# Kernel tuning notes

Measured on AMD Instinct MI355X. Metric: run time of the kernel, lower is better.

## Reference

```python
import jax, jax.numpy as jnp
import numpy as np

H = 16          # num_heads
WIN = 512       # window_size


def setup_inputs() -> dict:
    key = jax.random.key(0)
    ks = jax.random.split(key, 4)
    B, S, D = 1, 4096, 1024
    s = 1.0 / np.sqrt(D)
    x = jax.random.normal(ks[0], (B, S, D), jnp.float32)
    Wqkv = jax.random.normal(ks[1], (3 * D, D), jnp.float32) * s
    bqkv = jnp.zeros((3 * D,), jnp.float32)
    Wout = jax.random.normal(ks[2], (D, D), jnp.float32) * s
    bout = jnp.zeros((D,), jnp.float32)
    return {"x": x, "Wqkv": Wqkv, "bqkv": bqkv, "Wout": Wout, "bout": bout}


def reference(x, Wqkv, bqkv, Wout, bout):
    B, S, D = x.shape
    d = D // H
    pads = WIN // 2
    C = WIN                 # chunk of query tokens processed together
    N = S // C              # number of chunks
    L = C + WIN - 1         # key-block length covering all windows in a chunk

    qkv = (x @ Wqkv.T + bqkv).reshape(B, S, 3, H, d).transpose(2, 0, 3, 1, 4)
    q, k, v = qkv[0], qkv[1], qkv[2]          # [B,H,S,d]

    # zero-pad K/V exactly like F.pad(..., value=0.0) in the original
    kp = jnp.pad(k, ((0, 0), (0, 0), (pads, pads), (0, 0)))
    vp = jnp.pad(v, ((0, 0), (0, 0), (pads, pads), (0, 0)))

    # gather overlapping key/value blocks: chunk n covers padded idx [n*C, n*C+L)
    idx = jnp.arange(N)[:, None] * C + jnp.arange(L)[None, :]   # [N,L]
    kb = kp[:, :, idx, :]                      # [B,H,N,L,d]
    vb = vp[:, :, idx, :]
    qc = q.reshape(B, H, N, C, d)

    scores = jnp.einsum('bhncd,bhnld->bhncl', qc, kb) / np.sqrt(d).astype(np.float32)
    c = jnp.arange(C)[:, None]
    j = jnp.arange(L)[None, :]
    band = (j >= c) & (j < c + WIN)            # [C,L]; zero-pad keys stay IN (score 0), matching original
    scores = jnp.where(band, scores, -jnp.inf)
    attn = jax.nn.softmax(scores, axis=-1)

    o = jnp.einsum('bhncl,bhnld->bhncd', attn, vb).reshape(B, H, S, d)
    o = o.transpose(0, 2, 1, 3).reshape(B, S, D)
    return o @ Wout.T + bout
```

## Files before the change

kernel.cpp:

```cpp
#include <hip/hip_runtime.h>


typedef __bf16 bf16x8 __attribute__((ext_vector_type(8)));
typedef float f32x4 __attribute__((ext_vector_type(4)));
typedef unsigned short u16;
typedef unsigned int u32;

#define MFMA16(a, b, c) __builtin_amdgcn_mfma_f32_16x16x32_bf16(a, b, c, 0, 0, 0)

__device__ __forceinline__ u16 f2b(float f) {
  union { float f; u32 u; } x; x.f = f;
  u32 r = x.u + 0x7fffu + ((x.u >> 16) & 1u);
  return (u16)(r >> 16);
}

union U8x16 { int4 v; u16 u[8]; };

__device__ __forceinline__ void gll16(const u16* g, u16* l) {
  __builtin_amdgcn_global_load_lds(
      (const __attribute__((address_space(1))) u16*)g,
      (__attribute__((address_space(3))) u16*)l, 16, 0, 0);
}

__global__ void cvt_f32_bf16(const float* __restrict__ in, u16* __restrict__ out, int n8)
{
  const int i = blockIdx.x * blockDim.x + threadIdx.x;
  if (i >= n8) return;
  const float4 a = ((const float4*)in)[i * 2];
  const float4 b = ((const float4*)in)[i * 2 + 1];
  U8x16 t;
  t.u[0] = f2b(a.x); t.u[1] = f2b(a.y); t.u[2] = f2b(a.z); t.u[3] = f2b(a.w);
  t.u[4] = f2b(b.x); t.u[5] = f2b(b.y); t.u[6] = f2b(b.z); t.u[7] = f2b(b.w);
  ((int4*)out)[i] = t.v;
}

__global__ __launch_bounds__(256, 4) void gemm_qkv(
    const u16* __restrict__ A, const u16* __restrict__ B,
    const float* __restrict__ bias,
    u16* __restrict__ Qb, u16* __restrict__ Kp, u16* __restrict__ Vb)
{
  __shared__ u16 As[64 * 64];
  __shared__ u16 Bs[128 * 64];

  const int K = 1024;
  const int tid  = threadIdx.x;
  const int lane = tid & 63;
  const int wave = tid >> 6;
  const int quad = lane >> 4;
  const int c16  = lane & 15;
  const int wr   = wave >> 1;
  const int wc   = wave & 1;
  const long m0 = (long)blockIdx.y * 64;
  const long n0 = (long)blockIdx.x * 128;

  const int rowo   = lane >> 3;
  const int schunk = (lane & 7) ^ rowo;
  const u16* gA0 = &A[(m0 + wave * 16 + rowo) * K + schunk * 8];
  const u16* gA1 = gA0 + 8 * K;
  const u16* gB0 = &B[(n0 + wave * 32 + rowo) * K + schunk * 8];
  const u16* gB1 = gB0 + 8 * K;
  const u16* gB2 = gB0 + 16 * K;
  const u16* gB3 = gB0 + 24 * K;
  u16* const lA0 = &As[(wave * 16) * 64];
  u16* const lA1 = lA0 + 8 * 64;
  u16* const lB0 = &Bs[(wave * 32) * 64];
  u16* const lB1 = lB0 + 8 * 64;
  u16* const lB2 = lB0 + 16 * 64;
  u16* const lB3 = lB0 + 24 * 64;

  const int rsw = c16 & 7;
  const u16* pa[2][2]; const u16* pb[4][2];
#pragma unroll
  for (int i = 0; i < 2; ++i) {
    pa[i][0] = &As[(wr * 32 + i * 16 + c16) * 64 + (quad ^ rsw) * 8];
    pa[i][1] = &As[(wr * 32 + i * 16 + c16) * 64 + ((4 + quad) ^ rsw) * 8];
  }
#pragma unroll
  for (int j = 0; j < 4; ++j) {
    pb[j][0] = &Bs[(wc * 64 + j * 16 + c16) * 64 + (quad ^ rsw) * 8];
    pb[j][1] = &Bs[(wc * 64 + j * 16 + c16) * 64 + ((4 + quad) ^ rsw) * 8];
  }

  f32x4 acc[2][4];
#pragma unroll
  for (int i = 0; i < 2; ++i)
#pragma unroll
    for (int j = 0; j < 4; ++j)
      acc[i][j] = f32x4{0.f, 0.f, 0.f, 0.f};

  for (int k0 = 0; k0 < K; k0 += 64) {
    __syncthreads();
    gll16(gA0, lA0); gll16(gA1, lA1);
    gll16(gB0, lB0); gll16(gB1, lB1); gll16(gB2, lB2); gll16(gB3, lB3);
    gA0 += 64; gA1 += 64; gB0 += 64; gB1 += 64; gB2 += 64; gB3 += 64;
    __syncthreads();

#pragma unroll
    for (int h = 0; h < 2; ++h) {
      bf16x8 af[2], bfr[4];
#pragma unroll
      for (int i = 0; i < 2; ++i) af[i]  = *(const bf16x8*)pa[i][h];
#pragma unroll
      for (int j = 0; j < 4; ++j) bfr[j] = *(const bf16x8*)pb[j][h];
#pragma unroll
      for (int i = 0; i < 2; ++i)
#pragma unroll
        for (int j = 0; j < 4; ++j)
          acc[i][j] = MFMA16(af[i], bfr[j], acc[i][j]);
    }
  }

  const int region = (int)(n0 >> 10);
#pragma unroll
  for (int i = 0; i < 2; ++i) {
    const long row0 = m0 + wr * 32 + i * 16 + quad * 4;
#pragma unroll
    for (int j = 0; j < 4; ++j) {
      const long col = n0 + wc * 64 + j * 16 + c16;
      const float bv = bias[col];
#pragma unroll
      for (int r = 0; r < 4; ++r) {
        const u16 v = f2b(acc[i][j][r] + bv);
        const long row = row0 + r;
        if (region == 0) {
          Qb[row * 1024 + col] = v;
        } else if (region == 1) {
          const int n1 = (int)(col - 1024);
          const int h = n1 >> 6, d = n1 & 63;
          Kp[((long)h * 4608 + row + 256) * 64 + d] = v;
        } else {
          Vb[row * 1024 + (col - 2048)] = v;
        }
      }
    }
  }
}

__global__ __launch_bounds__(256, 4) void gemm_out(
    const u16* __restrict__ A, const u16* __restrict__ B,
    const float* __restrict__ bias, float* __restrict__ C)
{
  __shared__ u16 As[64 * 64];
  __shared__ u16 Bs[64 * 64];

  const int K = 1024, N = 1024;
  const int tid  = threadIdx.x;
  const int lane = tid & 63;
  const int wave = tid >> 6;
  const int quad = lane >> 4;
  const int c16  = lane & 15;
  const int wr   = wave >> 1;
  const int wc   = wave & 1;
  const long m0 = (long)blockIdx.y * 64;
  const long n0 = (long)blockIdx.x * 64;

  const int rowo   = lane >> 3;
  const int schunk = (lane & 7) ^ rowo;
  const u16* gA0 = &A[(m0 + wave * 16 + rowo) * K + schunk * 8];
  const u16* gA1 = gA0 + 8 * K;
  const u16* gB0 = &B[(n0 + wave * 16 + rowo) * K + schunk * 8];
  const u16* gB1 = gB0 + 8 * K;
  u16* const lA0 = &As[(wave * 16) * 64];
  u16* const lA1 = lA0 + 8 * 64;
  u16* const lB0 = &Bs[(wave * 16) * 64];
  u16* const lB1 = lB0 + 8 * 64;

  const int rsw = c16 & 7;
  const u16* pa[2][2]; const u16* pb[2][2];
#pragma unroll
  for (int i = 0; i < 2; ++i) {
    pa[i][0] = &As[(wr * 32 + i * 16 + c16) * 64 + (quad ^ rsw) * 8];
    pa[i][1] = &As[(wr * 32 + i * 16 + c16) * 64 + ((4 + quad) ^ rsw) * 8];
    pb[i][0] = &Bs[(wc * 32 + i * 16 + c16) * 64 + (quad ^ rsw) * 8];
    pb[i][1] = &Bs[(wc * 32 + i * 16 + c16) * 64 + ((4 + quad) ^ rsw) * 8];
  }

  f32x4 acc[2][2];
#pragma unroll
  for (int i = 0; i < 2; ++i)
#pragma unroll
    for (int j = 0; j < 2; ++j)
      acc[i][j] = f32x4{0.f, 0.f, 0.f, 0.f};

  for (int k0 = 0; k0 < K; k0 += 64) {
    __syncthreads();
    gll16(gA0, lA0); gll16(gA1, lA1);
    gll16(gB0, lB0); gll16(gB1, lB1);
    gA0 += 64; gA1 += 64; gB0 += 64; gB1 += 64;
    __syncthreads();

#pragma unroll
    for (int h = 0; h < 2; ++h) {
      bf16x8 af[2], bfr[2];
#pragma unroll
      for (int i = 0; i < 2; ++i) af[i]  = *(const bf16x8*)pa[i][h];
#pragma unroll
      for (int j = 0; j < 2; ++j) bfr[j] = *(const bf16x8*)pb[j][h];
#pragma unroll
      for (int i = 0; i < 2; ++i)
#pragma unroll
        for (int j = 0; j < 2; ++j)
          acc[i][j] = MFMA16(af[i], bfr[j], acc[i][j]);
    }
  }

#pragma unroll
  for (int i = 0; i < 2; ++i) {
    const long row0 = m0 + wr * 32 + i * 16 + quad * 4;
#pragma unroll
    for (int j = 0; j < 2; ++j) {
      const long col = n0 + wc * 32 + j * 16 + c16;
      const float bv = bias[col];
#pragma unroll
      for (int r = 0; r < 4; ++r)
        C[(row0 + r) * N + col] = acc[i][j][r] + bv;
    }
  }
}

__global__ __launch_bounds__(256, 2) void repack_v(
    const u16* __restrict__ Vb, u16* __restrict__ Kp, u16* __restrict__ VTp)
{
  __shared__ u16 lds[64 * 64];
  const int tile = blockIdx.x;
  const int h    = blockIdx.y;
  const int tid  = threadIdx.x;
  const int kt   = tile * 64 - 256;
  const long vtb = (long)h * 64 * 4608;

  if (kt < 0 || kt >= 4096) {
    const int4 z = {0, 0, 0, 0};
    for (int idx = tid; idx < 512; idx += 256) {
      const int r = idx >> 3, c = idx & 7;
      *(int4*)(&Kp[((long)h * 4608 + tile * 64 + r) * 64 + c * 8]) = z;
      *(int4*)(&VTp[vtb + (long)r * 4608 + tile * 64 + c * 8])     = z;
    }
    return;
  }

  for (int idx = tid; idx < 512; idx += 256) {
    const int r = idx >> 3, c = idx & 7;
    U8x16 t; t.v = *(const int4*)(&Vb[(long)(kt + r) * 1024 + h * 64 + c * 8]);
#pragma unroll
    for (int j = 0; j < 8; ++j) {
      const int d = c * 8 + j;
      lds[d * 64 + (((r >> 3) ^ ((c + j) & 7)) * 8) + (r & 7)] = t.u[j];
    }
  }
  __syncthreads();
  for (int idx = tid; idx < 512; idx += 256) {
    const int d = idx >> 3, c2 = idx & 7;
    const int sl = (c2 ^ ((d + (d >> 3)) & 7)) * 8;
    const int4 v = *(const int4*)(&lds[d * 64 + sl]);
    *(int4*)(&VTp[vtb + (long)d * 4608 + 256 + kt + c2 * 8]) = v;
  }
}

__global__ __launch_bounds__(256, 4) void swa_fused(
    const u16* __restrict__ Qb, const u16* __restrict__ Kp,
    const u16* __restrict__ VTp, u16* __restrict__ o)
{
  __shared__ u16 Ks[64 * 64];
  __shared__ u16 Vs[64 * 64];
  __shared__ u16 Ps[4 * 16 * 64];

  const int tid  = threadIdx.x;
  const int lane = tid & 63;
  const int w    = tid >> 6;
  const int quad = lane >> 4;
  const int c16  = lane & 15;
  const int h    = blockIdx.y;
  const int qb0  = blockIdx.x * 64;

  const long qrow = qb0 + w * 16 + c16;
  const bf16x8 aq0 = *(const bf16x8*)(&Qb[qrow * 1024 + h * 64 + quad * 8]);
  const bf16x8 aq1 = *(const bf16x8*)(&Qb[qrow * 1024 + h * 64 + 32 + quad * 8]);

  const int rowo   = lane >> 3;
  const int gchunk = (lane & 7) ^ rowo;
  const u16* gK0 = &Kp[((long)h * 4608 + qb0 + w * 16 + rowo) * 64 + gchunk * 8];
  const u16* gK1 = gK0 + 8 * 64;
  const u16* gV0 = &VTp[((long)h * 64 + w * 16 + rowo) * 4608 + qb0 + gchunk * 8];
  const u16* gV1 = gV0 + 8 * 4608;
  u16* const lK0 = &Ks[(w * 16) * 64];
  u16* const lK1 = lK0 + 8 * 64;
  u16* const lV0 = &Vs[(w * 16) * 64];
  u16* const lV1 = lV0 + 8 * 64;

  const int rsw = c16 & 7;
  const u16* pK[4][2]; const u16* pV[4][2];
#pragma unroll
  for (int t16 = 0; t16 < 4; ++t16) {
    pK[t16][0] = &Ks[(t16 * 16 + c16) * 64 + (quad ^ rsw) * 8];
    pK[t16][1] = &Ks[(t16 * 16 + c16) * 64 + ((4 + quad) ^ rsw) * 8];
    pV[t16][0] = &Vs[(t16 * 16 + c16) * 64 + (quad ^ rsw) * 8];
    pV[t16][1] = &Vs[(t16 * 16 + c16) * 64 + ((4 + quad) ^ rsw) * 8];
  }
  u16* const Pw  = &Ps[w * 1024];
  const u16* pP0 = &Ps[w * 1024 + c16 * 64 + (quad ^ rsw) * 8];
  const u16* pP1 = &Ps[w * 1024 + c16 * 64 + ((4 + quad) ^ rsw) * 8];

  const int dbase = c16 - 16 * w - quad * 4;

  f32x4 acc[4];
#pragma unroll
  for (int dt = 0; dt < 4; ++dt) acc[dt] = f32x4{0.f, 0.f, 0.f, 0.f};
  float rsum[4] = {0.f, 0.f, 0.f, 0.f};

  for (int t = 0; t < 9; ++t) {
    __syncthreads();
    gll16(gK0, lK0); gll16(gK1, lK1);
    gll16(gV0, lV0); gll16(gV1, lV1);
    gK0 += 64 * 64; gK1 += 64 * 64; gV0 += 64; gV1 += 64;
    __syncthreads();

#pragma unroll
    for (int tcol = 0; tcol < 4; ++tcol) {
      const bf16x8 bk0 = *(const bf16x8*)pK[tcol][0];
      const bf16x8 bk1 = *(const bf16x8*)pK[tcol][1];
      f32x4 s = f32x4{0.f, 0.f, 0.f, 0.f};
      s = MFMA16(aq0, bk0, s);
      s = MFMA16(aq1, bk1, s);
#pragma unroll
      for (int r = 0; r < 4; ++r) {
        const int delta = dbase + t * 64 + tcol * 16 - r;
        const float p = ((u32)delta < 512u) ? __expf(s[r] * 0.125f) : 0.f;
        rsum[r] += p;
        const int q  = quad * 4 + r;
        const int kc = tcol * 16 + c16;
        Pw[q * 64 + (((kc >> 3) ^ (q & 7)) * 8) + (kc & 7)] = f2b(p);
      }
    }

    const bf16x8 ap0 = *(const bf16x8*)pP0;
    const bf16x8 ap1 = *(const bf16x8*)pP1;
#pragma unroll
    for (int dt = 0; dt < 4; ++dt) {
      const bf16x8 bv0 = *(const bf16x8*)pV[dt][0];
      const bf16x8 bv1 = *(const bf16x8*)pV[dt][1];
      acc[dt] = MFMA16(ap0, bv0, acc[dt]);
      acc[dt] = MFMA16(ap1, bv1, acc[dt]);
    }
  }

#pragma unroll
  for (int off = 1; off < 16; off <<= 1)
#pragma unroll
    for (int r = 0; r < 4; ++r)
      rsum[r] += __shfl_xor(rsum[r], off, 64);

  const int qp = qb0 + w * 16 + quad * 4;
#pragma unroll
  for (int r = 0; r < 4; ++r) {
    const float inv = 1.f / rsum[r];
#pragma unroll
    for (int dt = 0; dt < 4; ++dt)
      o[(long)(qp + r) * 1024 + h * 64 + dt * 16 + c16] = f2b(acc[dt][r] * inv);
  }
}

extern "C" void kernel_launch(void* const* d_in, const int* in_sizes, int n_in,
                              void* d_out, int out_size, void* d_ws, size_t ws_size,
                              hipStream_t stream)
{
  const float* x    = (const float*)d_in[0];
  const float* Wqkv = (const float*)d_in[1];
  const float* bqkv = (const float*)d_in[2];
  const float* Wout = (const float*)d_in[3];
  const float* bout = (const float*)d_in[4];
  float* out = (float*)d_out;

  u16* xb    = (u16*)d_ws;
  u16* wqkvb = xb    + (size_t)4096 * 1024;
  u16* woutb = wqkvb + (size_t)3072 * 1024;
  u16* Qb    = woutb + (size_t)1024 * 1024;
  u16* Kp    = Qb    + (size_t)4096 * 1024;
  u16* VTp   = Kp    + (size_t)16 * 4608 * 64;
  u16* Vb    = VTp   + (size_t)16 * 4608 * 64;
  u16* o     = Vb;

  cvt_f32_bf16<<<4096 * 1024 / 8 / 256, 256, 0, stream>>>(x, xb, 4096 * 1024 / 8);
  cvt_f32_bf16<<<3072 * 1024 / 8 / 256, 256, 0, stream>>>(Wqkv, wqkvb, 3072 * 1024 / 8);
  cvt_f32_bf16<<<1024 * 1024 / 8 / 256, 256, 0, stream>>>(Wout, woutb, 1024 * 1024 / 8);

  gemm_qkv<<<dim3(3072 / 128, 4096 / 64), 256, 0, stream>>>(
      xb, wqkvb, bqkv, Qb, Kp, Vb);
  repack_v<<<dim3(72, 16), 256, 0, stream>>>(Vb, Kp, VTp);
  swa_fused<<<dim3(4096 / 64, 16), 256, 0, stream>>>(Qb, Kp, VTp, o);
  gemm_out<<<dim3(1024 / 64, 4096 / 64), 256, 0, stream>>>(o, woutb, bout, out);
}
```

Baseline: 167.0 us.

## Enlarge GEMM tiles and process 128 queries per attention block

The QKV GEMM moves to 128x128 block tiles with a 4x4 MFMA accumulator grid per wave. The output GEMM reuses the old 64x128 QKV tile shape. The attention kernel now handles 128 query rows per block (32 per wave), so each loaded K/V tile is shared by twice as many queries, and waves skip tiles outside their band. The aim is to cut global and LDS traffic per FLOP, at the cost of more registers (lower occupancy bound on gemm_qkv), a doubled P scratch buffer, and load imbalance across waves.

New measurement: 186.7 us. 11.8% more time.

```diff
diff --git a/kernel.cpp b/kernel.cpp
--- a/kernel.cpp
+++ b/kernel.cpp
@@ -34,15 +34,112 @@
   ((int4*)out)[i] = t.v;
 }
 
-__global__ __launch_bounds__(256, 4) void gemm_qkv(
+__global__ __launch_bounds__(256, 3) void gemm_qkv(
     const u16* __restrict__ A, const u16* __restrict__ B,
     const float* __restrict__ bias,
     u16* __restrict__ Qb, u16* __restrict__ Kp, u16* __restrict__ Vb)
 {
+  __shared__ u16 As[128 * 64];
+  __shared__ u16 Bs[128 * 64];
+
+  const int K = 1024;
+  const int tid  = threadIdx.x;
+  const int lane = tid & 63;
+  const int wave = tid >> 6;
+  const int quad = lane >> 4;
+  const int c16  = lane & 15;
+  const int wr   = wave >> 1;
+  const int wc   = wave & 1;
+  const long m0 = (long)blockIdx.y * 128;
+  const long n0 = (long)blockIdx.x * 128;
+
+  const int rowo   = lane >> 3;
+  const int schunk = (lane & 7) ^ rowo;
+  const u16* gA[4]; const u16* gB[4];
+  u16* lA[4]; u16* lB[4];
+#pragma unroll
+  for (int i = 0; i < 4; ++i) {
+    gA[i] = &A[(m0 + wave * 32 + i * 8 + rowo) * K + schunk * 8];
+    gB[i] = &B[(n0 + wave * 32 + i * 8 + rowo) * K + schunk * 8];
+    lA[i] = &As[(wave * 32 + i * 8) * 64];
+    lB[i] = &Bs[(wave * 32 + i * 8) * 64];
+  }
+
+  const int rsw  = c16 & 7;
+  const int off0 = (quad ^ rsw) * 8;
+  const int off1 = ((4 + quad) ^ rsw) * 8;
+  const u16* rA[4]; const u16* rB[4];
+#pragma unroll
+  for (int i = 0; i < 4; ++i) {
+    rA[i] = &As[(wr * 64 + i * 16 + c16) * 64];
+    rB[i] = &Bs[(wc * 64 + i * 16 + c16) * 64];
+  }
+
+  f32x4 acc[4][4];
+#pragma unroll
+  for (int i = 0; i < 4; ++i)
+#pragma unroll
+    for (int j = 0; j < 4; ++j)
+      acc[i][j] = f32x4{0.f, 0.f, 0.f, 0.f};
+
+  for (int k0 = 0; k0 < K; k0 += 64) {
+    __syncthreads();
+#pragma unroll
+    for (int i = 0; i < 4; ++i) { gll16(gA[i], lA[i]); gA[i] += 64; }
+#pragma unroll
+    for (int i = 0; i < 4; ++i) { gll16(gB[i], lB[i]); gB[i] += 64; }
+    __syncthreads();
+
+#pragma unroll
+    for (int h = 0; h < 2; ++h) {
+      const int off = h ? off1 : off0;
+      bf16x8 af[4], bfr[4];
+#pragma unroll
+      for (int i = 0; i < 4; ++i) af[i]  = *(const bf16x8*)(rA[i] + off);
+#pragma unroll
+      for (int j = 0; j < 4; ++j) bfr[j] = *(const bf16x8*)(rB[j] + off);
+#pragma unroll
+      for (int i = 0; i < 4; ++i)
+#pragma unroll
+        for (int j = 0; j < 4; ++j)
+          acc[i][j] = MFMA16(af[i], bfr[j], acc[i][j]);
+    }
+  }
+
+  const int region = (int)(n0 >> 10);
+#pragma unroll
+  for (int i = 0; i < 4; ++i) {
+    const long row0 = m0 + wr * 64 + i * 16 + quad * 4;
+#pragma unroll
+    for (int j = 0; j < 4; ++j) {
+      const long col = n0 + wc * 64 + j * 16 + c16;
+      const float bv = bias[col];
+#pragma unroll
+      for (int r = 0; r < 4; ++r) {
+        const u16 v = f2b(acc[i][j][r] + bv);
+        const long row = row0 + r;
+        if (region == 0) {
+          Qb[row * 1024 + col] = v;
+        } else if (region == 1) {
+          const int n1 = (int)(col - 1024);
+          const int h = n1 >> 6, d = n1 & 63;
+          Kp[((long)h * 4608 + row + 256) * 64 + d] = v;
+        } else {
+          Vb[row * 1024 + (col - 2048)] = v;
+        }
+      }
+    }
+  }
+}
+
+__global__ __launch_bounds__(256, 4) void gemm_out(
+    const u16* __restrict__ A, const u16* __restrict__ B,
+    const float* __restrict__ bias, float* __restrict__ C)
+{
   __shared__ u16 As[64 * 64];
   __shared__ u16 Bs[128 * 64];
 
-  const int K = 1024;
+  const int K = 1024, N = 1024;
   const int tid  = threadIdx.x;
   const int lane = tid & 63;
   const int wave = tid >> 6;
@@ -68,18 +165,14 @@
   u16* const lB2 = lB0 + 16 * 64;
   u16* const lB3 = lB0 + 24 * 64;
 
-  const int rsw = c16 & 7;
-  const u16* pa[2][2]; const u16* pb[4][2];
-#pragma unroll
-  for (int i = 0; i < 2; ++i) {
-    pa[i][0] = &As[(wr * 32 + i * 16 + c16) * 64 + (quad ^ rsw) * 8];
-    pa[i][1] = &As[(wr * 32 + i * 16 + c16) * 64 + ((4 + quad) ^ rsw) * 8];
-  }
-#pragma unroll
-  for (int j = 0; j < 4; ++j) {
-    pb[j][0] = &Bs[(wc * 64 + j * 16 + c16) * 64 + (quad ^ rsw) * 8];
-    pb[j][1] = &Bs[(wc * 64 + j * 16 + c16) * 64 + ((4 + quad) ^ rsw) * 8];
-  }
+  const int rsw  = c16 & 7;
+  const int off0 = (quad ^ rsw) * 8;
+  const int off1 = ((4 + quad) ^ rsw) * 8;
+  const u16* rA[2]; const u16* rB[4];
+#pragma unroll
+  for (int i = 0; i < 2; ++i) rA[i] = &As[(wr * 32 + i * 16 + c16) * 64];
+#pragma unroll
+  for (int j = 0; j < 4; ++j) rB[j] = &Bs[(wc * 64 + j * 16 + c16) * 64];
 
   f32x4 acc[2][4];
 #pragma unroll
@@ -97,11 +190,12 @@
 
 #pragma unroll
     for (int h = 0; h < 2; ++h) {
+      const int off = h ? off1 : off0;
       bf16x8 af[2], bfr[4];
 #pragma unroll
-      for (int i = 0; i < 2; ++i) af[i]  = *(const bf16x8*)pa[i][h];
-#pragma unroll
-      for (int j = 0; j < 4; ++j) bfr[j] = *(const bf16x8*)pb[j][h];
+      for (int i = 0; i < 2; ++i) af[i]  = *(const bf16x8*)(rA[i] + off);
+#pragma unroll
+      for (int j = 0; j < 4; ++j) bfr[j] = *(const bf16x8*)(rB[j] + off);
 #pragma unroll
       for (int i = 0; i < 2; ++i)
 #pragma unroll
@@ -110,106 +204,12 @@
     }
   }
 
-  const int region = (int)(n0 >> 10);
 #pragma unroll
   for (int i = 0; i < 2; ++i) {
     const long row0 = m0 + wr * 32 + i * 16 + quad * 4;
 #pragma unroll
     for (int j = 0; j < 4; ++j) {
       const long col = n0 + wc * 64 + j * 16 + c16;
-      const float bv = bias[col];
-#pragma unroll
-      for (int r = 0; r < 4; ++r) {
-        const u16 v = f2b(acc[i][j][r] + bv);
-        const long row = row0 + r;
-        if (region == 0) {
-          Qb[row * 1024 + col] = v;
-        } else if (region == 1) {
-          const int n1 = (int)(col - 1024);
-          const int h = n1 >> 6, d = n1 & 63;
-          Kp[((long)h * 4608 + row + 256) * 64 + d] = v;
-        } else {
-          Vb[row * 1024 + (col - 2048)] = v;
-        }
-      }
-    }
-  }
-}
-
-__global__ __launch_bounds__(256, 4) void gemm_out(
-    const u16* __restrict__ A, const u16* __restrict__ B,
-    const float* __restrict__ bias, float* __restrict__ C)
-{
-  __shared__ u16 As[64 * 64];
-  __shared__ u16 Bs[64 * 64];
-
-  const int K = 1024, N = 1024;
-  const int tid  = threadIdx.x;
-  const int lane = tid & 63;
-  const int wave = tid >> 6;
-  const int quad = lane >> 4;
-  const int c16  = lane & 15;
-  const int wr   = wave >> 1;
-  const int wc   = wave & 1;
-  const long m0 = (long)blockIdx.y * 64;
-  const long n0 = (long)blockIdx.x * 64;
-
-  const int rowo   = lane >> 3;
-  const int schunk = (lane & 7) ^ rowo;
-  const u16* gA0 = &A[(m0 + wave * 16 + rowo) * K + schunk * 8];
-  const u16* gA1 = gA0 + 8 * K;
-  const u16* gB0 = &B[(n0 + wave * 16 + rowo) * K + schunk * 8];
-  const u16* gB1 = gB0 + 8 * K;
-  u16* const lA0 = &As[(wave * 16) * 64];
-  u16* const lA1 = lA0 + 8 * 64;
-  u16* const lB0 = &Bs[(wave * 16) * 64];
-  u16* const lB1 = lB0 + 8 * 64;
-
-  const int rsw = c16 & 7;
-  const u16* pa[2][2]; const u16* pb[2][2];
-#pragma unroll
-  for (int i = 0; i < 2; ++i) {
-    pa[i][0] = &As[(wr * 32 + i * 16 + c16) * 64 + (quad ^ rsw) * 8];
-    pa[i][1] = &As[(wr * 32 + i * 16 + c16) * 64 + ((4 + quad) ^ rsw) * 8];
-    pb[i][0] = &Bs[(wc * 32 + i * 16 + c16) * 64 + (quad ^ rsw) * 8];
-    pb[i][1] = &Bs[(wc * 32 + i * 16 + c16) * 64 + ((4 + quad) ^ rsw) * 8];
-  }
-
-  f32x4 acc[2][2];
-#pragma unroll
-  for (int i = 0; i < 2; ++i)
-#pragma unroll
-    for (int j = 0; j < 2; ++j)
-      acc[i][j] = f32x4{0.f, 0.f, 0.f, 0.f};
-
-  for (int k0 = 0; k0 < K; k0 += 64) {
-    __syncthreads();
-    gll16(gA0, lA0); gll16(gA1, lA1);
-    gll16(gB0, lB0); gll16(gB1, lB1);
-    gA0 += 64; gA1 += 64; gB0 += 64; gB1 += 64;
-    __syncthreads();
-
-#pragma unroll
-    for (int h = 0; h < 2; ++h) {
-      bf16x8 af[2], bfr[2];
-#pragma unroll
-      for (int i = 0; i < 2; ++i) af[i]  = *(const bf16x8*)pa[i][h];
-#pragma unroll
-      for (int j = 0; j < 2; ++j) bfr[j] = *(const bf16x8*)pb[j][h];
-#pragma unroll
-      for (int i = 0; i < 2; ++i)
-#pragma unroll
-        for (int j = 0; j < 2; ++j)
-          acc[i][j] = MFMA16(af[i], bfr[j], acc[i][j]);
-    }
-  }
-
-#pragma unroll
-  for (int i = 0; i < 2; ++i) {
-    const long row0 = m0 + wr * 32 + i * 16 + quad * 4;
-#pragma unroll
-    for (int j = 0; j < 2; ++j) {
-      const long col = n0 + wc * 32 + j * 16 + c16;
       const float bv = bias[col];
 #pragma unroll
       for (int r = 0; r < 4; ++r)
@@ -262,7 +262,7 @@
 {
   __shared__ u16 Ks[64 * 64];
   __shared__ u16 Vs[64 * 64];
-  __shared__ u16 Ps[4 * 16 * 64];
+  __shared__ u16 Ps[4 * 32 * 64];
 
   const int tid  = threadIdx.x;
   const int lane = tid & 63;
@@ -270,11 +270,15 @@
   const int quad = lane >> 4;
   const int c16  = lane & 15;
   const int h    = blockIdx.y;
-  const int qb0  = blockIdx.x * 64;
-
-  const long qrow = qb0 + w * 16 + c16;
-  const bf16x8 aq0 = *(const bf16x8*)(&Qb[qrow * 1024 + h * 64 + quad * 8]);
-  const bf16x8 aq1 = *(const bf16x8*)(&Qb[qrow * 1024 + h * 64 + 32 + quad * 8]);
+  const int qb0  = blockIdx.x * 128;
+
+  bf16x8 aq[2][2];
+#pragma unroll
+  for (int qa = 0; qa < 2; ++qa) {
+    const long qrow = qb0 + w * 32 + qa * 16 + c16;
+    aq[qa][0] = *(const bf16x8*)(&Qb[qrow * 1024 + h * 64 + quad * 8]);
+    aq[qa][1] = *(const bf16x8*)(&Qb[qrow * 1024 + h * 64 + 32 + quad * 8]);
+  }
 
   const int rowo   = lane >> 3;
   const int gchunk = (lane & 7) ^ rowo;
@@ -287,75 +291,95 @@
   u16* const lV0 = &Vs[(w * 16) * 64];
   u16* const lV1 = lV0 + 8 * 64;
 
-  const int rsw = c16 & 7;
-  const u16* pK[4][2]; const u16* pV[4][2];
-#pragma unroll
-  for (int t16 = 0; t16 < 4; ++t16) {
-    pK[t16][0] = &Ks[(t16 * 16 + c16) * 64 + (quad ^ rsw) * 8];
-    pK[t16][1] = &Ks[(t16 * 16 + c16) * 64 + ((4 + quad) ^ rsw) * 8];
-    pV[t16][0] = &Vs[(t16 * 16 + c16) * 64 + (quad ^ rsw) * 8];
-    pV[t16][1] = &Vs[(t16 * 16 + c16) * 64 + ((4 + quad) ^ rsw) * 8];
-  }
-  u16* const Pw  = &Ps[w * 1024];
-  const u16* pP0 = &Ps[w * 1024 + c16 * 64 + (quad ^ rsw) * 8];
-  const u16* pP1 = &Ps[w * 1024 + c16 * 64 + ((4 + quad) ^ rsw) * 8];
-
-  const int dbase = c16 - 16 * w - quad * 4;
-
-  f32x4 acc[4];
-#pragma unroll
-  for (int dt = 0; dt < 4; ++dt) acc[dt] = f32x4{0.f, 0.f, 0.f, 0.f};
-  float rsum[4] = {0.f, 0.f, 0.f, 0.f};
-
-  for (int t = 0; t < 9; ++t) {
+  const int rsw  = c16 & 7;
+  const int off0 = (quad ^ rsw) * 8;
+  const int off1 = ((4 + quad) ^ rsw) * 8;
+  const u16* rK[4]; const u16* rV[4];
+#pragma unroll
+  for (int i = 0; i < 4; ++i) {
+    rK[i] = &Ks[(i * 16 + c16) * 64];
+    rV[i] = &Vs[(i * 16 + c16) * 64];
+  }
+  u16* const Pw = &Ps[w * 2048];
+  const u16* rP[2];
+#pragma unroll
+  for (int qa = 0; qa < 2; ++qa) rP[qa] = &Pw[(qa * 16 + c16) * 64];
+
+  const int t_lo = w >> 1;
+  const int t_hi = 8 + (w >> 1);
+  int dbase[2];
+#pragma unroll
+  for (int qa = 0; qa < 2; ++qa)
+    dbase[qa] = c16 - w * 32 - qa * 16 - quad * 4;
+
+  f32x4 acc[2][4];
+#pragma unroll
+  for (int qa = 0; qa < 2; ++qa)
+#pragma unroll
+    for (int dt = 0; dt < 4; ++dt) acc[qa][dt] = f32x4{0.f, 0.f, 0.f, 0.f};
+  float rsum[2][4] = {{0.f, 0.f, 0.f, 0.f}, {0.f, 0.f, 0.f, 0.f}};
+
+  for (int t = 0; t < 10; ++t) {
     __syncthreads();
     gll16(gK0, lK0); gll16(gK1, lK1);
     gll16(gV0, lV0); gll16(gV1, lV1);
     gK0 += 64 * 64; gK1 += 64 * 64; gV0 += 64; gV1 += 64;
     __syncthreads();
+    if (t < t_lo || t > t_hi) continue;
 
 #pragma unroll
     for (int tcol = 0; tcol < 4; ++tcol) {
-      const bf16x8 bk0 = *(const bf16x8*)pK[tcol][0];
-      const bf16x8 bk1 = *(const bf16x8*)pK[tcol][1];
-      f32x4 s = f32x4{0.f, 0.f, 0.f, 0.f};
-      s = MFMA16(aq0, bk0, s);
-      s = MFMA16(aq1, bk1, s);
-#pragma unroll
-      for (int r = 0; r < 4; ++r) {
-        const int delta = dbase + t * 64 + tcol * 16 - r;
-        const float p = ((u32)delta < 512u) ? __expf(s[r] * 0.125f) : 0.f;
-        rsum[r] += p;
-        const int q  = quad * 4 + r;
-        const int kc = tcol * 16 + c16;
-        Pw[q * 64 + (((kc >> 3) ^ (q & 7)) * 8) + (kc & 7)] = f2b(p);
+      const bf16x8 bk0 = *(const bf16x8*)(rK[tcol] + off0);
+      const bf16x8 bk1 = *(const bf16x8*)(rK[tcol] + off1);
+#pragma unroll
+      for (int qa = 0; qa < 2; ++qa) {
+        f32x4 s = f32x4{0.f, 0.f, 0.f, 0.f};
+        s = MFMA16(aq[qa][0], bk0, s);
+        s = MFMA16(aq[qa][1], bk1, s);
+#pragma unroll
+        for (int r = 0; r < 4; ++r) {
+          const int delta = dbase[qa] + t * 64 + tcol * 16 - r;
+          const float p = ((u32)delta < 512u) ? __expf(s[r] * 0.125f) : 0.f;
+          rsum[qa][r] += p;
+          const int qi = qa * 16 + quad * 4 + r;
+          const int kc = tcol * 16 + c16;
+          Pw[qi * 64 + (((kc >> 3) ^ (qi & 7)) * 8) + (kc & 7)] = f2b(p);
+        }
       }
     }
 
-    const bf16x8 ap0 = *(const bf16x8*)pP0;
-    const bf16x8 ap1 = *(const bf16x8*)pP1;
-#pragma unroll
-    for (int dt = 0; dt < 4; ++dt) {
-      const bf16x8 bv0 = *(const bf16x8*)pV[dt][0];
-      const bf16x8 bv1 = *(const bf16x8*)pV[dt][1];
-      acc[dt] = MFMA16(ap0, bv0, acc[dt]);
-      acc[dt] = MFMA16(ap1, bv1, acc[dt]);
+#pragma unroll
+    for (int qa = 0; qa < 2; ++qa) {
+      const bf16x8 ap0 = *(const bf16x8*)(rP[qa] + off0);
+      const bf16x8 ap1 = *(const bf16x8*)(rP[qa] + off1);
+#pragma unroll
+      for (int dt = 0; dt < 4; ++dt) {
+        const bf16x8 bv0 = *(const bf16x8*)(rV[dt] + off0);
+        const bf16x8 bv1 = *(const bf16x8*)(rV[dt] + off1);
+        acc[qa][dt] = MFMA16(ap0, bv0, acc[qa][dt]);
+        acc[qa][dt] = MFMA16(ap1, bv1, acc[qa][dt]);
+      }
     }
   }
 
 #pragma unroll
   for (int off = 1; off < 16; off <<= 1)
 #pragma unroll
-    for (int r = 0; r < 4; ++r)
-      rsum[r] += __shfl_xor(rsum[r], off, 64);
-
-  const int qp = qb0 + w * 16 + quad * 4;
-#pragma unroll
-  for (int r = 0; r < 4; ++r) {
-    const float inv = 1.f / rsum[r];
-#pragma unroll
-    for (int dt = 0; dt < 4; ++dt)
-      o[(long)(qp + r) * 1024 + h * 64 + dt * 16 + c16] = f2b(acc[dt][r] * inv);
+    for (int qa = 0; qa < 2; ++qa)
+#pragma unroll
+      for (int r = 0; r < 4; ++r)
+        rsum[qa][r] += __shfl_xor(rsum[qa][r], off, 64);
+
+#pragma unroll
+  for (int qa = 0; qa < 2; ++qa) {
+    const int qp = qb0 + w * 32 + qa * 16 + quad * 4;
+#pragma unroll
+    for (int r = 0; r < 4; ++r) {
+      const float inv = 1.f / rsum[qa][r];
+#pragma unroll
+      for (int dt = 0; dt < 4; ++dt)
+        o[(long)(qp + r) * 1024 + h * 64 + dt * 16 + c16] = f2b(acc[qa][dt][r] * inv);
+    }
   }
 }
 
@@ -383,9 +407,9 @@
   cvt_f32_bf16<<<3072 * 1024 / 8 / 256, 256, 0, stream>>>(Wqkv, wqkvb, 3072 * 1024 / 8);
   cvt_f32_bf16<<<1024 * 1024 / 8 / 256, 256, 0, stream>>>(Wout, woutb, 1024 * 1024 / 8);
 
-  gemm_qkv<<<dim3(3072 / 128, 4096 / 64), 256, 0, stream>>>(
+  gemm_qkv<<<dim3(3072 / 128, 4096 / 128), 256, 0, stream>>>(
       xb, wqkvb, bqkv, Qb, Kp, Vb);
   repack_v<<<dim3(72, 16), 256, 0, stream>>>(Vb, Kp, VTp);
-  swa_fused<<<dim3(4096 / 64, 16), 256, 0, stream>>>(Qb, Kp, VTp, o);
-  gemm_out<<<dim3(1024 / 64, 4096 / 64), 256, 0, stream>>>(o, woutb, bout, out);
-}
+  swa_fused<<<dim3(4096 / 128, 16), 256, 0, stream>>>(Qb, Kp, VTp, o);
+  gemm_out<<<dim3(1024 / 128, 4096 / 64), 256, 0, stream>>>(o, woutb, bout, out);
+}
```

## Shrink attention blocks to two waves, fuse conversions, trim LDS pointer registers

Applied to the files above, without the earlier changes.

The three fp32-to-bf16 conversion launches become a single kernel that picks its source buffer by index range. The sliding-window attention kernel now uses 32-query blocks of two waves, each wave loading four K/V row groups, which doubles the grid and halves the P scratch space. Across the GEMMs and attention, the precomputed per-half LDS pointers become one row pointer plus two shared offsets to save registers, and gemm_qkv's launch bound rises to 6 blocks per CU. The smaller attention blocks reload the same K/V tiles for half as many queries, so global and LDS traffic per query goes up in exchange for more parallelism and occupancy.

Result: slower. 190.9 us (+14.3%).

```diff
diff --git a/kernel.cpp b/kernel.cpp
--- a/kernel.cpp
+++ b/kernel.cpp
@@ -22,19 +22,23 @@
       (__attribute__((address_space(3))) u16*)l, 16, 0, 0);
 }
 
-__global__ void cvt_f32_bf16(const float* __restrict__ in, u16* __restrict__ out, int n8)
+__global__ void cvt_all(const float* __restrict__ x, const float* __restrict__ wqkv,
+                        const float* __restrict__ wout, u16* __restrict__ dst)
 {
   const int i = blockIdx.x * blockDim.x + threadIdx.x;
-  if (i >= n8) return;
-  const float4 a = ((const float4*)in)[i * 2];
-  const float4 b = ((const float4*)in)[i * 2 + 1];
+  const float* src; int off;
+  if (i < 524288)       { src = x;    off = i; }
+  else if (i < 917504)  { src = wqkv; off = i - 524288; }
+  else                  { src = wout; off = i - 917504; }
+  const float4 a = ((const float4*)src)[off * 2];
+  const float4 b = ((const float4*)src)[off * 2 + 1];
   U8x16 t;
   t.u[0] = f2b(a.x); t.u[1] = f2b(a.y); t.u[2] = f2b(a.z); t.u[3] = f2b(a.w);
   t.u[4] = f2b(b.x); t.u[5] = f2b(b.y); t.u[6] = f2b(b.z); t.u[7] = f2b(b.w);
-  ((int4*)out)[i] = t.v;
-}
-
-__global__ __launch_bounds__(256, 4) void gemm_qkv(
+  ((int4*)dst)[i] = t.v;
+}
+
+__global__ __launch_bounds__(256, 6) void gemm_qkv(
     const u16* __restrict__ A, const u16* __restrict__ B,
     const float* __restrict__ bias,
     u16* __restrict__ Qb, u16* __restrict__ Kp, u16* __restrict__ Vb)
@@ -68,18 +72,14 @@
   u16* const lB2 = lB0 + 16 * 64;
   u16* const lB3 = lB0 + 24 * 64;
 
-  const int rsw = c16 & 7;
-  const u16* pa[2][2]; const u16* pb[4][2];
-#pragma unroll
-  for (int i = 0; i < 2; ++i) {
-    pa[i][0] = &As[(wr * 32 + i * 16 + c16) * 64 + (quad ^ rsw) * 8];
-    pa[i][1] = &As[(wr * 32 + i * 16 + c16) * 64 + ((4 + quad) ^ rsw) * 8];
-  }
-#pragma unroll
-  for (int j = 0; j < 4; ++j) {
-    pb[j][0] = &Bs[(wc * 64 + j * 16 + c16) * 64 + (quad ^ rsw) * 8];
-    pb[j][1] = &Bs[(wc * 64 + j * 16 + c16) * 64 + ((4 + quad) ^ rsw) * 8];
-  }
+  const int rsw  = c16 & 7;
+  const int off0 = (quad ^ rsw) * 8;
+  const int off1 = ((4 + quad) ^ rsw) * 8;
+  const u16* rA[2]; const u16* rB[4];
+#pragma unroll
+  for (int i = 0; i < 2; ++i) rA[i] = &As[(wr * 32 + i * 16 + c16) * 64];
+#pragma unroll
+  for (int j = 0; j < 4; ++j) rB[j] = &Bs[(wc * 64 + j * 16 + c16) * 64];
 
   f32x4 acc[2][4];
 #pragma unroll
@@ -97,11 +97,12 @@
 
 #pragma unroll
     for (int h = 0; h < 2; ++h) {
+      const int off = h ? off1 : off0;
       bf16x8 af[2], bfr[4];
 #pragma unroll
-      for (int i = 0; i < 2; ++i) af[i]  = *(const bf16x8*)pa[i][h];
-#pragma unroll
-      for (int j = 0; j < 4; ++j) bfr[j] = *(const bf16x8*)pb[j][h];
+      for (int i = 0; i < 2; ++i) af[i]  = *(const bf16x8*)(rA[i] + off);
+#pragma unroll
+      for (int j = 0; j < 4; ++j) bfr[j] = *(const bf16x8*)(rB[j] + off);
 #pragma unroll
       for (int i = 0; i < 2; ++i)
 #pragma unroll
@@ -165,14 +166,14 @@
   u16* const lB0 = &Bs[(wave * 16) * 64];
   u16* const lB1 = lB0 + 8 * 64;
 
-  const int rsw = c16 & 7;
-  const u16* pa[2][2]; const u16* pb[2][2];
+  const int rsw  = c16 & 7;
+  const int off0 = (quad ^ rsw) * 8;
+  const int off1 = ((4 + quad) ^ rsw) * 8;
+  const u16* rA[2]; const u16* rB[2];
 #pragma unroll
   for (int i = 0; i < 2; ++i) {
-    pa[i][0] = &As[(wr * 32 + i * 16 + c16) * 64 + (quad ^ rsw) * 8];
-    pa[i][1] = &As[(wr * 32 + i * 16 + c16) * 64 + ((4 + quad) ^ rsw) * 8];
-    pb[i][0] = &Bs[(wc * 32 + i * 16 + c16) * 64 + (quad ^ rsw) * 8];
-    pb[i][1] = &Bs[(wc * 32 + i * 16 + c16) * 64 + ((4 + quad) ^ rsw) * 8];
+    rA[i] = &As[(wr * 32 + i * 16 + c16) * 64];
+    rB[i] = &Bs[(wc * 32 + i * 16 + c16) * 64];
   }
 
   f32x4 acc[2][2];
@@ -191,11 +192,12 @@
 
 #pragma unroll
     for (int h = 0; h < 2; ++h) {
+      const int off = h ? off1 : off0;
       bf16x8 af[2], bfr[2];
 #pragma unroll
-      for (int i = 0; i < 2; ++i) af[i]  = *(const bf16x8*)pa[i][h];
-#pragma unroll
-      for (int j = 0; j < 2; ++j) bfr[j] = *(const bf16x8*)pb[j][h];
+      for (int i = 0; i < 2; ++i) af[i]  = *(const bf16x8*)(rA[i] + off);
+#pragma unroll
+      for (int j = 0; j < 2; ++j) bfr[j] = *(const bf16x8*)(rB[j] + off);
 #pragma unroll
       for (int i = 0; i < 2; ++i)
 #pragma unroll
@@ -256,13 +258,13 @@
   }
 }
 
-__global__ __launch_bounds__(256, 4) void swa_fused(
+__global__ __launch_bounds__(128, 4) void swa_fused(
     const u16* __restrict__ Qb, const u16* __restrict__ Kp,
     const u16* __restrict__ VTp, u16* __restrict__ o)
 {
   __shared__ u16 Ks[64 * 64];
   __shared__ u16 Vs[64 * 64];
-  __shared__ u16 Ps[4 * 16 * 64];
+  __shared__ u16 Ps[2 * 16 * 64];
 
   const int tid  = threadIdx.x;
   const int lane = tid & 63;
@@ -270,7 +272,7 @@
   const int quad = lane >> 4;
   const int c16  = lane & 15;
   const int h    = blockIdx.y;
-  const int qb0  = blockIdx.x * 64;
+  const int qb0  = blockIdx.x * 32;
 
   const long qrow = qb0 + w * 16 + c16;
   const bf16x8 aq0 = *(const bf16x8*)(&Qb[qrow * 1024 + h * 64 + quad * 8]);
@@ -278,27 +280,27 @@
 
   const int rowo   = lane >> 3;
   const int gchunk = (lane & 7) ^ rowo;
-  const u16* gK0 = &Kp[((long)h * 4608 + qb0 + w * 16 + rowo) * 64 + gchunk * 8];
-  const u16* gK1 = gK0 + 8 * 64;
-  const u16* gV0 = &VTp[((long)h * 64 + w * 16 + rowo) * 4608 + qb0 + gchunk * 8];
-  const u16* gV1 = gV0 + 8 * 4608;
-  u16* const lK0 = &Ks[(w * 16) * 64];
-  u16* const lK1 = lK0 + 8 * 64;
-  u16* const lV0 = &Vs[(w * 16) * 64];
-  u16* const lV1 = lV0 + 8 * 64;
-
-  const int rsw = c16 & 7;
-  const u16* pK[4][2]; const u16* pV[4][2];
-#pragma unroll
-  for (int t16 = 0; t16 < 4; ++t16) {
-    pK[t16][0] = &Ks[(t16 * 16 + c16) * 64 + (quad ^ rsw) * 8];
-    pK[t16][1] = &Ks[(t16 * 16 + c16) * 64 + ((4 + quad) ^ rsw) * 8];
-    pV[t16][0] = &Vs[(t16 * 16 + c16) * 64 + (quad ^ rsw) * 8];
-    pV[t16][1] = &Vs[(t16 * 16 + c16) * 64 + ((4 + quad) ^ rsw) * 8];
-  }
-  u16* const Pw  = &Ps[w * 1024];
-  const u16* pP0 = &Ps[w * 1024 + c16 * 64 + (quad ^ rsw) * 8];
-  const u16* pP1 = &Ps[w * 1024 + c16 * 64 + ((4 + quad) ^ rsw) * 8];
+  const u16* gK[4]; const u16* gV[4];
+  u16* lK[4]; u16* lV[4];
+#pragma unroll
+  for (int i = 0; i < 4; ++i) {
+    gK[i] = &Kp[((long)h * 4608 + qb0 + w * 32 + i * 8 + rowo) * 64 + gchunk * 8];
+    gV[i] = &VTp[((long)h * 64 + w * 32 + i * 8 + rowo) * 4608 + qb0 + gchunk * 8];
+    lK[i] = &Ks[(w * 32 + i * 8) * 64];
+    lV[i] = &Vs[(w * 32 + i * 8) * 64];
+  }
+
+  const int rsw  = c16 & 7;
+  const int off0 = (quad ^ rsw) * 8;
+  const int off1 = ((4 + quad) ^ rsw) * 8;
+  const u16* rK[4]; const u16* rV[4];
+#pragma unroll
+  for (int i = 0; i < 4; ++i) {
+    rK[i] = &Ks[(i * 16 + c16) * 64];
+    rV[i] = &Vs[(i * 16 + c16) * 64];
+  }
+  u16* const Pw = &Ps[w * 1024];
+  const u16* rP = &Pw[c16 * 64];
 
   const int dbase = c16 - 16 * w - quad * 4;
 
@@ -309,15 +311,16 @@
 
   for (int t = 0; t < 9; ++t) {
     __syncthreads();
-    gll16(gK0, lK0); gll16(gK1, lK1);
-    gll16(gV0, lV0); gll16(gV1, lV1);
-    gK0 += 64 * 64; gK1 += 64 * 64; gV0 += 64; gV1 += 64;
+#pragma unroll
+    for (int i = 0; i < 4; ++i) { gll16(gK[i], lK[i]); gK[i] += 64 * 64; }
+#pragma unroll
+    for (int i = 0; i < 4; ++i) { gll16(gV[i], lV[i]); gV[i] += 64; }
     __syncthreads();
 
 #pragma unroll
     for (int tcol = 0; tcol < 4; ++tcol) {
-      const bf16x8 bk0 = *(const bf16x8*)pK[tcol][0];
-      const bf16x8 bk1 = *(const bf16x8*)pK[tcol][1];
+      const bf16x8 bk0 = *(const bf16x8*)(rK[tcol] + off0);
+      const bf16x8 bk1 = *(const bf16x8*)(rK[tcol] + off1);
       f32x4 s = f32x4{0.f, 0.f, 0.f, 0.f};
       s = MFMA16(aq0, bk0, s);
       s = MFMA16(aq1, bk1, s);
@@ -326,18 +329,18 @@
         const int delta = dbase + t * 64 + tcol * 16 - r;
         const float p = ((u32)delta < 512u) ? __expf(s[r] * 0.125f) : 0.f;
         rsum[r] += p;
-        const int q  = quad * 4 + r;
+        const int qi = quad * 4 + r;
         const int kc = tcol * 16 + c16;
-        Pw[q * 64 + (((kc >> 3) ^ (q & 7)) * 8) + (kc & 7)] = f2b(p);
+        Pw[qi * 64 + (((kc >> 3) ^ (qi & 7)) * 8) + (kc & 7)] = f2b(p);
       }
     }
 
-    const bf16x8 ap0 = *(const bf16x8*)pP0;
-    const bf16x8 ap1 = *(const bf16x8*)pP1;
+    const bf16x8 ap0 = *(const bf16x8*)(rP + off0);
+    const bf16x8 ap1 = *(const bf16x8*)(rP + off1);
 #pragma unroll
     for (int dt = 0; dt < 4; ++dt) {
-      const bf16x8 bv0 = *(const bf16x8*)pV[dt][0];
-      const bf16x8 bv1 = *(const bf16x8*)pV[dt][1];
+      const bf16x8 bv0 = *(const bf16x8*)(rV[dt] + off0);
+      const bf16x8 bv1 = *(const bf16x8*)(rV[dt] + off1);
       acc[dt] = MFMA16(ap0, bv0, acc[dt]);
       acc[dt] = MFMA16(ap1, bv1, acc[dt]);
     }
@@ -379,13 +382,11 @@
   u16* Vb    = VTp   + (size_t)16 * 4608 * 64;
   u16* o     = Vb;
 
-  cvt_f32_bf16<<<4096 * 1024 / 8 / 256, 256, 0, stream>>>(x, xb, 4096 * 1024 / 8);
-  cvt_f32_bf16<<<3072 * 1024 / 8 / 256, 256, 0, stream>>>(Wqkv, wqkvb, 3072 * 1024 / 8);
-  cvt_f32_bf16<<<1024 * 1024 / 8 / 256, 256, 0, stream>>>(Wout, woutb, 1024 * 1024 / 8);
+  cvt_all<<<1048576 / 256, 256, 0, stream>>>(x, Wqkv, Wout, xb);
 
   gemm_qkv<<<dim3(3072 / 128, 4096 / 64), 256, 0, stream>>>(
       xb, wqkvb, bqkv, Qb, Kp, Vb);
   repack_v<<<dim3(72, 16), 256, 0, stream>>>(Vb, Kp, VTp);
-  swa_fused<<<dim3(4096 / 64, 16), 256, 0, stream>>>(Qb, Kp, VTp, o);
+  swa_fused<<<dim3(4096 / 32, 16), 128, 0, stream>>>(Qb, Kp, VTp, o);
   gemm_out<<<dim3(1024 / 64, 4096 / 64), 256, 0, stream>>>(o, woutb, bout, out);
 }
```
